# Kernel tuning notes

Measured on AMD Instinct MI355X. Metric: run time of the kernel, lower is better.

Reference implementation:

```python
import jax, jax.numpy as jnp
import numpy as np

# ---- static config (from search_space / module defaults) ----
B, NCG = 4096, 2                 # batch of archs, cell groups
NUM_INIT, NUM_NODE_INPUTS, NUM_STEPS = 2, 2, 4
NUM_NODES = NUM_INIT + NUM_STEPS  # 6
N_EDGE = NUM_NODE_INPUTS * NUM_STEPS  # 8
NUM_OPS = 7                      # 'none' is index 0
NONE_INDEX = 0
NODE_DIM = OP_DIM = HIDDEN = 48
GCN_DIMS = [128, 128]


def _uniform(key, shape, fan_in):
    s = 1.0 / np.sqrt(fan_in)
    return jax.random.uniform(key, shape, minval=-s, maxval=s, dtype=jnp.float32)


def setup_inputs() -> dict:
    key = jax.random.key(0)
    ks = jax.random.split(key, 14)
    # from-node for step i must be < NUM_INIT + i -> per-edge maxval [2,2,3,3,4,4,5,5]
    fmax = jnp.repeat(jnp.arange(NUM_INIT, NUM_NODES), NUM_NODE_INPUTS)
    f_nodes = jax.random.randint(ks[0], (B, NCG, N_EDGE), 0, fmax)
    ops = jax.random.randint(ks[1], (B, NCG, N_EDGE), 0, NUM_OPS)
    archs = jnp.stack([f_nodes, ops], axis=2).astype(jnp.int32)  # (B,NCG,2,E)

    init_node_emb = jax.random.normal(ks[2], (NCG, NUM_INIT, NODE_DIM), dtype=jnp.float32)
    other_node_emb = jnp.zeros((NCG, 1, NODE_DIM), dtype=jnp.float32)  # zero-init, trainable
    # op embeddings; 'none' op (idx 0) is frozen zeros
    op_embs = jax.random.normal(ks[3], (NUM_OPS, OP_DIM), dtype=jnp.float32).at[NONE_INDEX].set(0.0)

    Wx = _uniform(ks[4], (NODE_DIM, HIDDEN), NODE_DIM)
    bx = _uniform(ks[5], (HIDDEN,), NODE_DIM)
    W1 = _uniform(ks[6], (HIDDEN, GCN_DIMS[0]), GCN_DIMS[0])
    Wa1 = _uniform(ks[7], (OP_DIM, GCN_DIMS[0]), OP_DIM)
    ba1 = _uniform(ks[8], (GCN_DIMS[0],), OP_DIM)
    W2 = _uniform(ks[9], (GCN_DIMS[0], GCN_DIMS[1]), GCN_DIMS[1])
    Wa2 = _uniform(ks[10], (OP_DIM, GCN_DIMS[1]), OP_DIM)
    ba2 = _uniform(ks[11], (GCN_DIMS[1],), OP_DIM)
    return {"archs": archs, "init_node_emb": init_node_emb, "other_node_emb": other_node_emb,
            "op_embs": op_embs, "Wx": Wx, "bx": bx, "W1": W1, "Wa1": Wa1, "ba1": ba1,
            "W2": W2, "Wa2": Wa2, "ba2": ba2}


def _build_adj_ops(archs):
    """Dense adjacency (edge counts) and per-input-slot op-index matrices."""
    f = archs[:, :, 0, :].reshape(-1, N_EDGE)    # (B*NCG, E) from-nodes
    ops = archs[:, :, 1, :].reshape(-1, N_EDGE)  # (B*NCG, E) op ids
    t = jnp.repeat(jnp.arange(NUM_INIT, NUM_NODES), NUM_NODE_INPUTS)  # (E,) to-nodes
    Bt = B * NCG
    b_idx = jnp.arange(Bt)[:, None]
    adj = jnp.zeros((Bt, NUM_NODES, NUM_NODES), jnp.float32)
    adj = adj.at[b_idx, t[None, :], f].add(1.0)
    adj_op_inds = []
    for k in range(NUM_NODE_INPUTS):
        fk, tk, opk = f[:, k::NUM_NODE_INPUTS], t[k::NUM_NODE_INPUTS], ops[:, k::NUM_NODE_INPUTS]
        aoi = jnp.full((Bt, NUM_NODES, NUM_NODES), NONE_INDEX, dtype=jnp.int32)
        aoi = aoi.at[b_idx, tk[None, :], fk].set(opk)  # (t,f) unique within a slot
        adj_op_inds.append(aoi.reshape(B, NCG, NUM_NODES, NUM_NODES))
    return adj.reshape(B, NCG, NUM_NODES, NUM_NODES), adj_op_inds


def _gcn_layer(y, adj_op_inds, op_embs, W, Wa, ba):
    """DenseGraphOpEdgeFlow (defaults: attention, no plus_I/normalize/bias):
    out_i = support_i + sum_slots sum_j sigmoid(att(op_emb[op_ij])) * 1[op_ij != none] * support_j
    """
    support = y @ W                                   # (B,CG,N,out)
    out = support
    for aoi in adj_op_inds:
        attn = jax.nn.sigmoid(op_embs[aoi] @ Wa + ba)  # (B,CG,N,N,out)
        attn = attn * (aoi != NONE_INDEX)[..., None].astype(support.dtype)
        out = out + jnp.einsum('bcijo,bcjo->bcio', attn, support)
    return out


def reference(archs, init_node_emb, other_node_emb, op_embs, Wx, bx,
              W1, Wa1, ba1, W2, Wa2, ba2):
    _adj, adj_op_inds = _build_adj_ops(archs)  # adj counts unused under default gcn_kwargs
    node = jnp.concatenate([
        jnp.broadcast_to(init_node_emb[None], (B, NCG, NUM_INIT, NODE_DIM)),
        jnp.broadcast_to(other_node_emb[None], (B, NCG, NUM_STEPS, NODE_DIM))], axis=2)
    y = node @ Wx + bx                                 # x_hidden
    y = _gcn_layer(y, adj_op_inds, op_embs, W1, Wa1, ba1)
    y = jax.nn.relu(y)                                 # relu between layers
    y = _gcn_layer(y, adj_op_inds, op_embs, W2, Wa2, ba2)
    y = y[:, :, NUM_INIT:, :].mean(axis=2)             # drop init nodes, mean over steps
    return y.reshape(B, -1)                            # (B, NCG*128)
```

## Files before the change

kernel.cpp:

```cpp
#include <hip/hip_runtime.h>

#define NPAIR 8192

#define NCFG_REAL 5292
#define NCFG      5296
#define CPER      2646
#define WS_AT2F   0
#define WS_TAB    1024
#define WS_NEED   ((size_t)(1024 + NCFG * 128) * 4)

#define COMP4(v, j) ((j) == 0 ? (v).x : (j) == 1 ? (v).y : (j) == 2 ? (v).z : (v).w)

__device__ __forceinline__ float sigmoidf_(float x) {
  return 1.0f / (1.0f + __expf(-x));
}

__global__ __launch_bounds__(256) void config_kernel(
    const float* __restrict__ init_emb, const float* __restrict__ other_emb,
    const float* __restrict__ op_embs,  const float* __restrict__ Wx,
    const float* __restrict__ bx,       const float* __restrict__ W1,
    const float* __restrict__ Wa1,      const float* __restrict__ ba1,
    const float* __restrict__ W2,       const float* __restrict__ Wa2,
    const float* __restrict__ ba2,      float* __restrict__ ws)
{
  __shared__ __align__(16) float wsh[6144];
  __shared__ __align__(16) float s1sh[1536];
  __shared__ __align__(16) float at1sh[896];
  __shared__ __align__(16) float at2sh[896];
  __shared__ __align__(16) float y0[576];
  const int t = threadIdx.x;

  for (int i = t; i < 576; i += 256) ((float4*)wsh)[i] = ((const float4*)Wx)[i];
  if (t < 48)       ((float4*)at2sh)[t] = ((const float4*)init_emb)[t];
  else if (t < 72)  ((float4*)at2sh)[t] = ((const float4*)other_emb)[t - 48];
  else if (t < 84)  ((float4*)at2sh)[t] = ((const float4*)bx)[t - 72];
  __syncthreads();

  for (int idx = t; idx < 576; idx += 256) {
    int c = idx / 288, i = (idx / 48) % 6, h = idx % 48;
    const float* nptr = (i < 2) ? (at2sh + (c * 2 + i) * 48)
                                : (at2sh + 192 + c * 48);
    float acc = at2sh[288 + h];
    for (int d = 0; d < 48; ++d) acc += nptr[d] * wsh[d * 48 + h];
    y0[idx] = acc;
  }
  __syncthreads();

  for (int i = t; i < 1536; i += 256) ((float4*)wsh)[i] = ((const float4*)W1)[i];
  __syncthreads();
  for (int idx = t; idx < 1536; idx += 256) {
    int ci = idx >> 7, o = idx & 127;
    const float* yp = y0 + ci * 48;
    float acc = 0.f;
    for (int h = 0; h < 48; ++h) acc += yp[h] * wsh[h * 128 + o];
    s1sh[idx] = acc;
  }
  __syncthreads();

  for (int i = t; i < 1536; i += 256) ((float4*)wsh)[i] = ((const float4*)Wa1)[i];
  if (t < 84) ((float4*)y0)[t] = ((const float4*)op_embs)[t];
  __syncthreads();
  for (int idx = t; idx < 896; idx += 256) {
    int op = idx >> 7, o = idx & 127;
    float a = ba1[o];
    for (int d = 0; d < 48; ++d) a += y0[op * 48 + d] * wsh[d * 128 + o];
    at1sh[idx] = a;
  }
  __syncthreads();

  for (int i = t; i < 1536; i += 256) ((float4*)wsh)[i] = ((const float4*)Wa2)[i];
  __syncthreads();
  for (int idx = t; idx < 896; idx += 256) {
    int op = idx >> 7, o = idx & 127;
    float a2 = ba2[o];
    for (int d = 0; d < 48; ++d) a2 += y0[op * 48 + d] * wsh[d * 128 + o];
    float v1 = (op == 0) ? 0.f : sigmoidf_(at1sh[idx]);
    float v2 = (op == 0) ? 0.f : sigmoidf_(a2);
    at1sh[idx] = v1;
    at2sh[idx] = v2;
    ws[WS_AT2F + idx] = v2;
  }
  __syncthreads();

  const int w  = t >> 6, o2 = t & 63;
  const int cfg0 = blockIdx.x * 16 + w * 4;
  const float2* s1f = (const float2*)s1sh;
  const float2* a1f = (const float2*)at1sh;
  float* y1p = wsh + w * 512;

  #pragma unroll
  for (int r = 0; r < 4; ++r) {
    int cfg = cfg0 + r;
    float2 v;
    if (cfg < NCFG_REAL) {
      int c = cfg / CPER, q = cfg % CPER;
      int i, b;
      if (q < 196)       { i = 2; b = 0; }
      else if (q < 637)  { i = 3; b = 196; }
      else if (q < 1421) { i = 4; b = 637; }
      else               { i = 5; b = 1421; }
      q -= b;
      int op2_ = q % 7; q /= 7;
      int f2_  = q % i; q /= i;
      int op1_ = q % 7;
      int f1_  = q / 7;
      int cb = c * 384;
      v = s1f[cb + i * 64 + o2];
      float2 A0 = a1f[op1_ * 64 + o2], B0 = s1f[cb + f1_ * 64 + o2];
      float2 A1 = a1f[op2_ * 64 + o2], B1 = s1f[cb + f2_ * 64 + o2];
      v.x += A0.x * B0.x + A1.x * B1.x;
      v.y += A0.y * B0.y + A1.y * B1.y;
    } else {
      int j = cfg - NCFG_REAL, c = j >> 1, i = j & 1;
      v = s1f[c * 384 + i * 64 + o2];
    }
    ((float2*)(y1p + r * 128))[o2] =
        make_float2(fmaxf(v.x, 0.f), fmaxf(v.y, 0.f));
  }
  __syncthreads();

  const float2* W2f = (const float2*)W2;
  float ax0 = 0, ax1 = 0, ax2 = 0, ax3 = 0;
  float ay0 = 0, ay1 = 0, ay2 = 0, ay3 = 0;

  for (int h = 0; h < 128; h += 4) {
    float4 q0 = *(const float4*)(y1p + 0 * 128 + h);
    float4 q1 = *(const float4*)(y1p + 1 * 128 + h);
    float4 q2 = *(const float4*)(y1p + 2 * 128 + h);
    float4 q3 = *(const float4*)(y1p + 3 * 128 + h);
    #pragma unroll
    for (int j = 0; j < 4; ++j) {
      float2 wf = W2f[(h + j) * 64 + o2];
      float w0 = wf.x, w1 = wf.y, y;
      y = COMP4(q0, j); ax0 += y * w0; ay0 += y * w1;
      y = COMP4(q1, j); ax1 += y * w0; ay1 += y * w1;
      y = COMP4(q2, j); ax2 += y * w0; ay2 += y * w1;
      y = COMP4(q3, j); ax3 += y * w0; ay3 += y * w1;
    }
  }

  float2* tab = (float2*)(ws + WS_TAB);
  tab[(cfg0 + 0) * 64 + o2] = make_float2(ax0, ay0);
  tab[(cfg0 + 1) * 64 + o2] = make_float2(ax1, ay1);
  tab[(cfg0 + 2) * 64 + o2] = make_float2(ax2, ay2);
  tab[(cfg0 + 3) * 64 + o2] = make_float2(ax3, ay3);
}

__global__ __launch_bounds__(256) void gather_kernel(
    const int* __restrict__ archs, const float* __restrict__ ws,
    float* __restrict__ out)
{
  const int t  = threadIdx.x;
  const int pp = t >> 6;
  const int o2 = t & 63;
  const int P  = blockIdx.x * 4 + pp;
  const int c  = P & 1;

  __shared__ int archsh[64];
  if (t < 64) archsh[t] = archs[blockIdx.x * 64 + t];
  __syncthreads();

  int f[8], op[8];
  #pragma unroll
  for (int e = 0; e < 8; ++e) { f[e] = archsh[pp * 16 + e]; op[e] = archsh[pp * 16 + 8 + e]; }

  const float2* tab = (const float2*)(ws + WS_TAB);
  const float2* a2f = (const float2*)(ws + WS_AT2F);

  float2 S0 = tab[(NCFG_REAL + c * 2 + 0) * 64 + o2];
  float2 S1 = tab[(NCFG_REAL + c * 2 + 1) * 64 + o2];
  float2 S2, S3, S4, S5;
  {
    const int ib[4] = {0, 196, 637, 1421};
    #pragma unroll
    for (int i = 2; i < 6; ++i) {
      int e0 = 2 * (i - 2), e1 = e0 + 1;
      int cid = c * CPER + ib[i - 2] +
                ((f[e0] * 7 + op[e0]) * i + f[e1]) * 7 + op[e1];
      float2 v = tab[cid * 64 + o2];
      if (i == 2) S2 = v; else if (i == 3) S3 = v;
      else if (i == 4) S4 = v; else S5 = v;
    }
  }
  float2 A2[8];
  #pragma unroll
  for (int e = 0; e < 8; ++e) A2[e] = a2f[op[e] * 64 + o2];

  float r0 = S2.x + S3.x + S4.x + S5.x;
  float r1 = S2.y + S3.y + S4.y + S5.y;
  #pragma unroll
  for (int e = 0; e < 8; ++e) {
    int fe = f[e];
    float sx, sy;
    if (fe == 0)      { sx = S0.x; sy = S0.y; }
    else if (fe == 1) { sx = S1.x; sy = S1.y; }
    else if (fe == 2) { sx = S2.x; sy = S2.y; }
    else if (fe == 3) { sx = S3.x; sy = S3.y; }
    else              { sx = S4.x; sy = S4.y; }
    r0 += A2[e].x * sx;
    r1 += A2[e].y * sy;
  }
  ((float2*)out)[P * 64 + o2] = make_float2(r0 * 0.25f, r1 * 0.25f);
}

#define FB_S1   0
#define FB_AT1  1536
#define FB_AT2  2432
#define FB_S2I  3328

__global__ __launch_bounds__(512) void precompute_kernel(
    const float* __restrict__ init_emb, const float* __restrict__ other_emb,
    const float* __restrict__ op_embs,  const float* __restrict__ Wx,
    const float* __restrict__ bx,       const float* __restrict__ W1,
    const float* __restrict__ Wa1,      const float* __restrict__ ba1,
    const float* __restrict__ W2,       const float* __restrict__ Wa2,
    const float* __restrict__ ba2,      float* __restrict__ ws)
{
  const int t   = threadIdx.x;
  const int blk = blockIdx.x;
  __shared__ float y0[576];
  __shared__ float s1sh[1536];
  for (int idx = t; idx < 576; idx += 512) {
    int c = idx / 288, i = (idx / 48) % 6, h = idx % 48;
    const float* nptr = (i < 2) ? (init_emb + (c * 2 + i) * 48)
                                : (other_emb + c * 48);
    float acc = bx[h];
    for (int d = 0; d < 48; ++d) acc += nptr[d] * Wx[d * 48 + h];
    y0[idx] = acc;
  }
  __syncthreads();
  for (int idx = t; idx < 1536; idx += 512) {
    int ci = idx >> 7, o = idx & 127;
    const float* yp = y0 + ci * 48;
    float acc = 0.f;
    for (int h = 0; h < 48; ++h) acc += yp[h] * W1[h * 128 + o];
    s1sh[idx] = acc;
    ws[FB_S1 + idx] = acc;
  }
  for (int idx = blk * 112 + t; idx < (blk + 1) * 112; idx += 512) {
    int op = idx >> 7, o = idx & 127;
    float a1 = ba1[o], a2 = ba2[o];
    for (int d = 0; d < 48; ++d) {
      float e = op_embs[op * 48 + d];
      a1 += e * Wa1[d * 128 + o];
      a2 += e * Wa2[d * 128 + o];
    }
    ws[FB_AT1 + idx] = (op == 0) ? 0.f : sigmoidf_(a1);
    ws[FB_AT2 + idx] = (op == 0) ? 0.f : sigmoidf_(a2);
  }
  __syncthreads();
  for (int idx = blk * 64 + t; idx < (blk + 1) * 64; idx += 512) {
    int c = idx >> 8, i = (idx >> 7) & 1, o = idx & 127;
    const float* sp = s1sh + (c * 6 + i) * 128;
    float acc = 0.f;
    for (int h = 0; h < 128; ++h) acc += fmaxf(sp[h], 0.f) * W2[h * 128 + o];
    ws[FB_S2I + idx] = acc;
  }
}

__global__ __launch_bounds__(256) void main_kernel(
    const int* __restrict__ archs, const float* __restrict__ W2,
    const float* __restrict__ ws, float* __restrict__ out)
{
  const int t  = threadIdx.x;
  const int pp = t >> 6;
  const int o2 = t & 63;
  const int P  = blockIdx.x * 4 + pp;
  const int c  = P & 1;
  __shared__ float y1sh[4][512];
  __shared__ int   archsh[64];
  if (t < 64) archsh[t] = archs[blockIdx.x * 64 + t];
  __syncthreads();
  int f[8], op[8];
  #pragma unroll
  for (int e = 0; e < 8; ++e) { f[e] = archsh[pp * 16 + e]; op[e] = archsh[pp * 16 + 8 + e]; }
  const float2* s1p = (const float2*)ws + c * 384;
  const float2* at1 = (const float2*)(ws + FB_AT1);
  const float2* at2 = (const float2*)(ws + FB_AT2);
  const float2* s2i = (const float2*)(ws + FB_S2I) + c * 128;
  float2 A2[8];
  #pragma unroll
  for (int e = 0; e < 8; ++e) A2[e] = at2[op[e] * 64 + o2];
  float2 S0 = s2i[o2], S1 = s2i[64 + o2];
  #pragma unroll
  for (int i = 0; i < 4; ++i) {
    float2 v = s1p[(2 + i) * 64 + o2];
    int e0 = 2 * i, e1 = 2 * i + 1;
    float2 A0 = at1[op[e0] * 64 + o2];
    float2 B0 = s1p[f[e0] * 64 + o2];
    float2 A1 = at1[op[e1] * 64 + o2];
    float2 B1 = s1p[f[e1] * 64 + o2];
    v.x += A0.x * B0.x + A1.x * B1.x;
    v.y += A0.y * B0.y + A1.y * B1.y;
    ((float2*)(y1sh[pp] + i * 128))[o2] =
        make_float2(fmaxf(v.x, 0.f), fmaxf(v.y, 0.f));
  }
  __syncthreads();
  const float* y1p = y1sh[pp];
  const float2* W2f = (const float2*)W2;
  float ax0 = 0, ax1 = 0, ax2 = 0, ax3 = 0;
  float ay0 = 0, ay1 = 0, ay2 = 0, ay3 = 0;
  for (int h = 0; h < 128; h += 4) {
    float4 q0 = *(const float4*)(y1p + 0 * 128 + h);
    float4 q1 = *(const float4*)(y1p + 1 * 128 + h);
    float4 q2 = *(const float4*)(y1p + 2 * 128 + h);
    float4 q3 = *(const float4*)(y1p + 3 * 128 + h);
    #pragma unroll
    for (int j = 0; j < 4; ++j) {
      float2 wf = W2f[(h + j) * 64 + o2];
      float w0 = wf.x, w1 = wf.y, y;
      y = COMP4(q0, j); ax0 += y * w0; ay0 += y * w1;
      y = COMP4(q1, j); ax1 += y * w0; ay1 += y * w1;
      y = COMP4(q2, j); ax2 += y * w0; ay2 += y * w1;
      y = COMP4(q3, j); ax3 += y * w0; ay3 += y * w1;
    }
  }
  float r0 = ax0 + ax1 + ax2 + ax3;
  float r1 = ay0 + ay1 + ay2 + ay3;
  #pragma unroll
  for (int e = 0; e < 8; ++e) {
    int fe = f[e];
    float sx, sy;
    if (fe == 0)      { sx = S0.x; sy = S0.y; }
    else if (fe == 1) { sx = S1.x; sy = S1.y; }
    else if (fe == 2) { sx = ax0; sy = ay0; }
    else if (fe == 3) { sx = ax1; sy = ay1; }
    else if (fe == 4) { sx = ax2; sy = ay2; }
    else              { sx = ax3; sy = ay3; }
    r0 += A2[e].x * sx;
    r1 += A2[e].y * sy;
  }
  ((float2*)out)[P * 64 + o2] = make_float2(r0 * 0.25f, r1 * 0.25f);
}

extern "C" void kernel_launch(void* const* d_in, const int* in_sizes, int n_in,
                              void* d_out, int out_size, void* d_ws, size_t ws_size,
                              hipStream_t stream) {
  const int* archs = (const int*)d_in[0];
  float* ws = (float*)d_ws;
  if (ws_size >= WS_NEED) {
    config_kernel<<<331, 256, 0, stream>>>(
        (const float*)d_in[1], (const float*)d_in[2], (const float*)d_in[3],
        (const float*)d_in[4], (const float*)d_in[5], (const float*)d_in[6],
        (const float*)d_in[7], (const float*)d_in[8], (const float*)d_in[9],
        (const float*)d_in[10], (const float*)d_in[11], ws);
    gather_kernel<<<NPAIR / 4, 256, 0, stream>>>(archs, ws, (float*)d_out);
  } else {
    precompute_kernel<<<8, 512, 0, stream>>>(
        (const float*)d_in[1], (const float*)d_in[2], (const float*)d_in[3],
        (const float*)d_in[4], (const float*)d_in[5], (const float*)d_in[6],
        (const float*)d_in[7], (const float*)d_in[8], (const float*)d_in[9],
        (const float*)d_in[10], (const float*)d_in[11], ws);
    main_kernel<<<NPAIR / 4, 256, 0, stream>>>(archs, (const float*)d_in[9], ws,
                                               (float*)d_out);
  }
}
```

Before: 103.1 us.

## Fuse config and gather kernels into one cooperative kernel with grid sync

```diff
diff --git a/kernel.cpp b/kernel.cpp
--- a/kernel.cpp
+++ b/kernel.cpp
@@ -1,4 +1,7 @@
 #include <hip/hip_runtime.h>
+#include <hip/hip_cooperative_groups.h>
+
+namespace cg = cooperative_groups;
 
 #define NPAIR 8192
 
@@ -13,6 +16,203 @@
 
 __device__ __forceinline__ float sigmoidf_(float x) {
   return 1.0f / (1.0f + __expf(-x));
+}
+
+__global__ __launch_bounds__(256, 2) void fused_kernel(
+    const float* __restrict__ init_emb, const float* __restrict__ other_emb,
+    const float* __restrict__ op_embs,  const float* __restrict__ Wx,
+    const float* __restrict__ bx,       const float* __restrict__ W1,
+    const float* __restrict__ Wa1,      const float* __restrict__ ba1,
+    const float* __restrict__ W2,       const float* __restrict__ Wa2,
+    const float* __restrict__ ba2,      const int* __restrict__ archs,
+    float* __restrict__ ws,             float* __restrict__ out)
+{
+  __shared__ __align__(16) float wsh[6144];
+  __shared__ __align__(16) float s1sh[1536];
+  __shared__ __align__(16) float at1sh[896];
+  __shared__ __align__(16) float at2sh[896];
+  __shared__ __align__(16) float y0[576];
+  const int t = threadIdx.x;
+
+  if (blockIdx.x < 331) {
+    for (int i = t; i < 576; i += 256) ((float4*)wsh)[i] = ((const float4*)Wx)[i];
+    if (t < 48)       ((float4*)at2sh)[t] = ((const float4*)init_emb)[t];
+    else if (t < 72)  ((float4*)at2sh)[t] = ((const float4*)other_emb)[t - 48];
+    else if (t < 84)  ((float4*)at2sh)[t] = ((const float4*)bx)[t - 72];
+    __syncthreads();
+
+    for (int idx = t; idx < 576; idx += 256) {
+      int c = idx / 288, i = (idx / 48) % 6, h = idx % 48;
+      const float* nptr = (i < 2) ? (at2sh + (c * 2 + i) * 48)
+                                  : (at2sh + 192 + c * 48);
+      float acc = at2sh[288 + h];
+      for (int d = 0; d < 48; ++d) acc += nptr[d] * wsh[d * 48 + h];
+      y0[idx] = acc;
+    }
+    __syncthreads();
+
+    for (int i = t; i < 1536; i += 256) ((float4*)wsh)[i] = ((const float4*)W1)[i];
+    __syncthreads();
+    for (int idx = t; idx < 1536; idx += 256) {
+      int ci = idx >> 7, o = idx & 127;
+      const float* yp = y0 + ci * 48;
+      float acc = 0.f;
+      for (int h = 0; h < 48; ++h) acc += yp[h] * wsh[h * 128 + o];
+      s1sh[idx] = acc;
+    }
+    __syncthreads();
+
+    for (int i = t; i < 1536; i += 256) ((float4*)wsh)[i] = ((const float4*)Wa1)[i];
+    if (t < 84) ((float4*)y0)[t] = ((const float4*)op_embs)[t];
+    __syncthreads();
+    for (int idx = t; idx < 896; idx += 256) {
+      int op = idx >> 7, o = idx & 127;
+      float a = ba1[o];
+      for (int d = 0; d < 48; ++d) a += y0[op * 48 + d] * wsh[d * 128 + o];
+      at1sh[idx] = a;
+    }
+    __syncthreads();
+
+    for (int i = t; i < 1536; i += 256) ((float4*)wsh)[i] = ((const float4*)Wa2)[i];
+    __syncthreads();
+    for (int idx = t; idx < 896; idx += 256) {
+      int op = idx >> 7, o = idx & 127;
+      float a2 = ba2[o];
+      for (int d = 0; d < 48; ++d) a2 += y0[op * 48 + d] * wsh[d * 128 + o];
+      float v1 = (op == 0) ? 0.f : sigmoidf_(at1sh[idx]);
+      float v2 = (op == 0) ? 0.f : sigmoidf_(a2);
+      at1sh[idx] = v1;
+      at2sh[idx] = v2;
+      ws[WS_AT2F + idx] = v2;
+    }
+    __syncthreads();
+
+    const int w  = t >> 6, o2 = t & 63;
+    const int cfg0 = blockIdx.x * 16 + w * 4;
+    const float2* s1f = (const float2*)s1sh;
+    const float2* a1f = (const float2*)at1sh;
+    float* y1p = wsh + w * 512;
+
+    #pragma unroll
+    for (int r = 0; r < 4; ++r) {
+      int cfg = cfg0 + r;
+      float2 v;
+      if (cfg < NCFG_REAL) {
+        int c = cfg / CPER, q = cfg % CPER;
+        int i, b;
+        if (q < 196)       { i = 2; b = 0; }
+        else if (q < 637)  { i = 3; b = 196; }
+        else if (q < 1421) { i = 4; b = 637; }
+        else               { i = 5; b = 1421; }
+        q -= b;
+        int op2_ = q % 7; q /= 7;
+        int f2_  = q % i; q /= i;
+        int op1_ = q % 7;
+        int f1_  = q / 7;
+        int cb = c * 384;
+        v = s1f[cb + i * 64 + o2];
+        float2 A0 = a1f[op1_ * 64 + o2], B0 = s1f[cb + f1_ * 64 + o2];
+        float2 A1 = a1f[op2_ * 64 + o2], B1 = s1f[cb + f2_ * 64 + o2];
+        v.x += A0.x * B0.x + A1.x * B1.x;
+        v.y += A0.y * B0.y + A1.y * B1.y;
+      } else {
+        int j = cfg - NCFG_REAL, c = j >> 1, i = j & 1;
+        v = s1f[c * 384 + i * 64 + o2];
+      }
+      ((float2*)(y1p + r * 128))[o2] =
+          make_float2(fmaxf(v.x, 0.f), fmaxf(v.y, 0.f));
+    }
+    __syncthreads();
+
+    const float2* W2f = (const float2*)W2;
+    float ax0 = 0, ax1 = 0, ax2 = 0, ax3 = 0;
+    float ay0 = 0, ay1 = 0, ay2 = 0, ay3 = 0;
+
+    for (int h = 0; h < 128; h += 4) {
+      float4 q0 = *(const float4*)(y1p + 0 * 128 + h);
+      float4 q1 = *(const float4*)(y1p + 1 * 128 + h);
+      float4 q2 = *(const float4*)(y1p + 2 * 128 + h);
+      float4 q3 = *(const float4*)(y1p + 3 * 128 + h);
+      #pragma unroll
+      for (int j = 0; j < 4; ++j) {
+        float2 wf = W2f[(h + j) * 64 + o2];
+        float w0 = wf.x, w1 = wf.y, y;
+        y = COMP4(q0, j); ax0 += y * w0; ay0 += y * w1;
+        y = COMP4(q1, j); ax1 += y * w0; ay1 += y * w1;
+        y = COMP4(q2, j); ax2 += y * w0; ay2 += y * w1;
+        y = COMP4(q3, j); ax3 += y * w0; ay3 += y * w1;
+      }
+    }
+
+    float2* tab = (float2*)(ws + WS_TAB);
+    tab[(cfg0 + 0) * 64 + o2] = make_float2(ax0, ay0);
+    tab[(cfg0 + 1) * 64 + o2] = make_float2(ax1, ay1);
+    tab[(cfg0 + 2) * 64 + o2] = make_float2(ax2, ay2);
+    tab[(cfg0 + 3) * 64 + o2] = make_float2(ax3, ay3);
+  }
+
+  __threadfence();
+  cg::this_grid().sync();
+  __syncthreads();
+
+  {
+    int* archsh = (int*)wsh;
+    archsh[t] = archs[blockIdx.x * 256 + t];
+    __syncthreads();
+
+    const int pp = t >> 6;
+    const int o2 = t & 63;
+    const int c = pp & 1;
+
+    const float2* tab = (const float2*)(ws + WS_TAB);
+    const float2* a2f = (const float2*)(ws + WS_AT2F);
+
+    const float2 S0 = tab[(NCFG_REAL + c * 2 + 0) * 64 + o2];
+    const float2 S1 = tab[(NCFG_REAL + c * 2 + 1) * 64 + o2];
+
+    #pragma unroll
+    for (int g4 = 0; g4 < 4; ++g4) {
+      const int P    = blockIdx.x * 16 + g4 * 4 + pp;
+      const int base = g4 * 64 + pp * 16;
+
+      int f[8], op[8];
+      #pragma unroll
+      for (int e = 0; e < 8; ++e) { f[e] = archsh[base + e]; op[e] = archsh[base + 8 + e]; }
+
+      float2 S2, S3, S4, S5;
+      {
+        const int ib[4] = {0, 196, 637, 1421};
+        #pragma unroll
+        for (int i = 2; i < 6; ++i) {
+          int e0 = 2 * (i - 2), e1 = e0 + 1;
+          int cid = c * CPER + ib[i - 2] +
+                    ((f[e0] * 7 + op[e0]) * i + f[e1]) * 7 + op[e1];
+          float2 v = tab[cid * 64 + o2];
+          if (i == 2) S2 = v; else if (i == 3) S3 = v;
+          else if (i == 4) S4 = v; else S5 = v;
+        }
+      }
+      float2 A2[8];
+      #pragma unroll
+      for (int e = 0; e < 8; ++e) A2[e] = a2f[op[e] * 64 + o2];
+
+      float r0 = S2.x + S3.x + S4.x + S5.x;
+      float r1 = S2.y + S3.y + S4.y + S5.y;
+      #pragma unroll
+      for (int e = 0; e < 8; ++e) {
+        int fe = f[e];
+        float sx, sy;
+        if (fe == 0)      { sx = S0.x; sy = S0.y; }
+        else if (fe == 1) { sx = S1.x; sy = S1.y; }
+        else if (fe == 2) { sx = S2.x; sy = S2.y; }
+        else if (fe == 3) { sx = S3.x; sy = S3.y; }
+        else              { sx = S4.x; sy = S4.y; }
+        r0 += A2[e].x * sx;
+        r1 += A2[e].y * sy;
+      }
+      ((float2*)out)[P * 64 + o2] = make_float2(r0 * 0.25f, r1 * 0.25f);
+    }
+  }
 }
 
 __global__ __launch_bounds__(256) void config_kernel(
@@ -339,12 +539,32 @@
   const int* archs = (const int*)d_in[0];
   float* ws = (float*)d_ws;
   if (ws_size >= WS_NEED) {
-    config_kernel<<<331, 256, 0, stream>>>(
-        (const float*)d_in[1], (const float*)d_in[2], (const float*)d_in[3],
-        (const float*)d_in[4], (const float*)d_in[5], (const float*)d_in[6],
-        (const float*)d_in[7], (const float*)d_in[8], (const float*)d_in[9],
-        (const float*)d_in[10], (const float*)d_in[11], ws);
-    gather_kernel<<<NPAIR / 4, 256, 0, stream>>>(archs, ws, (float*)d_out);
+    const float* init_emb  = (const float*)d_in[1];
+    const float* other_emb = (const float*)d_in[2];
+    const float* op_embs   = (const float*)d_in[3];
+    const float* Wx_  = (const float*)d_in[4];
+    const float* bx_  = (const float*)d_in[5];
+    const float* W1_  = (const float*)d_in[6];
+    const float* Wa1_ = (const float*)d_in[7];
+    const float* ba1_ = (const float*)d_in[8];
+    const float* W2_  = (const float*)d_in[9];
+    const float* Wa2_ = (const float*)d_in[10];
+    const float* ba2_ = (const float*)d_in[11];
+    float* out_ = (float*)d_out;
+
+    void* args[] = {(void*)&init_emb, (void*)&other_emb, (void*)&op_embs,
+                    (void*)&Wx_,  (void*)&bx_,  (void*)&W1_,  (void*)&Wa1_,
+                    (void*)&ba1_, (void*)&W2_,  (void*)&Wa2_, (void*)&ba2_,
+                    (void*)&archs, (void*)&ws,  (void*)&out_};
+    hipError_t err = hipLaunchCooperativeKernel(
+        (const void*)fused_kernel, dim3(512), dim3(256), args, 0, stream);
+    if (err != hipSuccess) {
+      (void)hipGetLastError();
+      config_kernel<<<331, 256, 0, stream>>>(
+          init_emb, other_emb, op_embs, Wx_, bx_, W1_, Wa1_, ba1_, W2_, Wa2_,
+          ba2_, ws);
+      gather_kernel<<<NPAIR / 4, 256, 0, stream>>>(archs, ws, (float*)d_out);
+    }
   } else {
     precompute_kernel<<<8, 512, 0, stream>>>(
         (const float*)d_in[1], (const float*)d_in[2], (const float*)d_in[3],
```

After: 235.7 us. 2.28x slower.
